# Kernel tuning notes

Measured on AMD Instinct MI355X. Metric: run time of the kernel, lower is better.

## Reference

```python
import jax, jax.numpy as jnp
import numpy as np

# Module hyperparameters (from init_kwargs)
LEARNING_RATE = 0.01  # not used inside compute_weight_update
TAU_PLUS = 20.0
TAU_MINUS = 20.0
A_PLUS = 0.005
A_MINUS = 0.00525
TARGET_RATE = 0.1
HOMEOSTATIC_RATE = 0.001
TAU_HOMEOSTATIC = 1000.0

B, T, N_PRE, N_POST = 16, 8192, 128, 128


def setup_inputs() -> dict:
    key = jax.random.key(0)
    k1, k2, k3 = jax.random.split(key, 3)
    # Bernoulli spike trains at ~target_rate firing probability
    pre_spikes = (jax.random.uniform(k1, (B, T, N_PRE)) < TARGET_RATE).astype(jnp.float32)
    post_spikes = (jax.random.uniform(k2, (B, T, N_POST)) < TARGET_RATE).astype(jnp.float32)
    weights = jax.random.uniform(k3, (N_PRE, N_POST), dtype=jnp.float32)
    return {"pre_spikes": pre_spikes, "post_spikes": post_spikes, "weights": weights, "dt": 1}


def _temporal_corr(x, kernel, pad):
    """Correlate x [B,T,N] along time with 1-D kernel [L], padding pad=(lo,hi)."""
    b, t, n = x.shape
    xr = jnp.moveaxis(x, 1, 2).reshape(b * n, 1, t)  # [B*N, 1, T]
    k = kernel.reshape(1, 1, -1).astype(x.dtype)
    y = jax.lax.conv_general_dilated(
        xr, k, window_strides=(1,), padding=[pad],
        dimension_numbers=("NCH", "OIH", "NCH"))
    return jnp.moveaxis(y.reshape(b, n, t), 2, 1)  # [B,T,N]


def reference(pre_spikes, post_spikes, weights, dt):
    b, t, n_pre = pre_spikes.shape
    dt = float(dt)

    # Homeostatic rate tracking (first call: avg rates initialized to target_rate)
    alpha = dt / TAU_HOMEOSTATIC
    current_post_rate = post_spikes.mean(axis=(0, 1))
    avg_post_rate = (1.0 - alpha) * TARGET_RATE + alpha * current_post_rate

    # Truncated exponential STDP window: tau in 1..min(int(3*tau)-1, ...) = 1..59
    L = int(TAU_PLUS * 3)  # 60 taps (tau=0 tap zeroed)
    taus = jnp.arange(L, dtype=jnp.float32)
    w_plus = jnp.where(taus > 0, A_PLUS * jnp.exp(-taus * dt / TAU_PLUS), 0.0)
    w_minus = jnp.where(taus > 0, A_MINUS * jnp.exp(-taus * dt / TAU_MINUS), 0.0)

    # LTP: post_filt[t] = sum_{tau>=1} w_plus[tau] * post[t+tau] (future, zero-padded)
    post_filt = _temporal_corr(post_spikes, w_plus, (0, L - 1))
    # LTD: pre_filt[t] = sum_{tau>=1} w_minus[tau] * pre[t-tau] (past, zero-padded)
    pre_filt = _temporal_corr(pre_spikes, w_minus[::-1], (L - 1, 0))

    # sum_t mean_b outer(pre[t], post_filt[t]) - outer(pre_filt[t], post[t]), then /T
    ltp = jnp.einsum("btp,btq->pq", pre_spikes, post_filt)
    ltd = jnp.einsum("btp,btq->pq", pre_filt, post_spikes)
    stdp_update = (ltp - ltd) / (b * t)

    # Homeostatic regulation pulls post rate toward target
    post_rate_error = avg_post_rate - TARGET_RATE
    homeostatic_update = -HOMEOSTATIC_RATE * post_rate_error[None, :] * weights

    return stdp_update + homeostatic_update
```

## Files before the change

kernel.cpp:

```cpp
#include <hip/hip_runtime.h>

#define BB 16
#define TT 8192
#define NN 128
constexpr int CHUNK = 256;
constexpr int NBLK  = BB * TT / CHUNK;
constexpr int OUTN  = NN * NN;
constexpr int GS    = 264;
constexpr int SLOTS = OUTN / 2;
constexpr int PROWS = 315;

typedef _Float16 f16x8 __attribute__((ext_vector_type(8)));
typedef _Float16 f16x2 __attribute__((ext_vector_type(2)));
typedef float    f32x4 __attribute__((ext_vector_type(4)));

__device__ __forceinline__ unsigned short h16(float x) {
    _Float16 h = (_Float16)x;
    return __builtin_bit_cast(unsigned short, h);
}
__device__ __forceinline__ unsigned int pack2(float x, float y) {
    return (unsigned int)h16(x) | ((unsigned int)h16(y) << 16);
}
__device__ __forceinline__ float2 ldL(const unsigned short* p_lds, int m, int q0) {
    const unsigned int v = *(const unsigned int*)&p_lds[m * NN + q0];
    const f16x2 h = __builtin_bit_cast(f16x2, v);
    return make_float2((float)h[0], (float)h[1]);
}

template<bool ATOMIC>
__global__ __launch_bounds__(512, 4)
void stdp_main(const float* __restrict__ pre, const float* __restrict__ post,
               const int* __restrict__ dtp,
               unsigned int* __restrict__ part, float* __restrict__ wpost,
               float* __restrict__ outat)
{
    __shared__ __align__(16) char smem[PROWS * NN * 2];
    unsigned short* post_lds = (unsigned short*)smem;
    unsigned short* g_lds    = (unsigned short*)smem;
    float*          lds_ps   = (float*)(smem + NN * GS * 2);

    const int tid   = threadIdx.x;
    const int blk   = blockIdx.x;
    const int b     = blk >> 5;
    const int chunk = blk & 31;
    const int t0    = chunk * CHUNK;
    const int wv    = tid >> 6;
    const int lane  = tid & 63;

    const float dtf = (float)(*dtp);
    const float r   = expf(-dtf * (1.0f / 20.0f));

    const float* pb = post + (size_t)b * TT * NN;
    const float* ab = pre  + (size_t)b * TT * NN;

    {
        const int c  = tid & 31;
        const int mr = tid >> 5;
        for (int m = mr; m < PROWS; m += 16) {
            const int t = t0 + 1 + m;
            float4 v = make_float4(0.f, 0.f, 0.f, 0.f);
            if (t < TT) v = *(const float4*)(pb + (size_t)t * NN + c * 4);
            *(uint2*)&post_lds[m * NN + c * 4] = make_uint2(pack2(v.x, v.y), pack2(v.z, v.w));
        }
    }
    __syncthreads();

    const int win  = wv;
    const int q0   = lane * 2;
    const int base = win * 32;
    float ps0 = 0.f, ps1 = 0.f;

    unsigned int pk0[16], pk1[16];
    {
        float2 p  = ldL(post_lds, base + 31, q0);
        float wt  = r;
        float gx = r * p.x, gy = r * p.y;
        ps0 += p.x; ps1 += p.y;
        #pragma unroll
        for (int tau = 2; tau <= 59; ++tau) {
            wt *= r;
            p = ldL(post_lds, base + 30 + tau, q0);
            gx = fmaf(wt, p.x, gx);
            gy = fmaf(wt, p.y, gy);
        }
        const float r60 = wt * r;
        pk0[15] = (unsigned int)h16(gx) << 16;
        pk1[15] = (unsigned int)h16(gy) << 16;
        #pragma unroll
        for (int c = 30; c >= 0; --c) {
            const float2 p1  = ldL(post_lds, base + c,      q0);
            const float2 p60 = ldL(post_lds, base + c + 59, q0);
            gx = r * (gx + p1.x) - r60 * p60.x;
            gy = r * (gy + p1.y) - r60 * p60.y;
            ps0 += p1.x; ps1 += p1.y;
            if (c & 1) {
                pk0[c >> 1] = (unsigned int)h16(gx) << 16;
                pk1[c >> 1] = (unsigned int)h16(gy) << 16;
            } else {
                pk0[c >> 1] |= h16(gx);
                pk1[c >> 1] |= h16(gy);
            }
        }
    }
    __syncthreads();

    {
        unsigned short* d0 = &g_lds[q0 * GS + win * 32];
        unsigned short* d1 = &g_lds[(q0 + 1) * GS + win * 32];
        #pragma unroll
        for (int s = 0; s < 4; ++s) {
            *(uint4*)(d0 + 8 * s) = make_uint4(pk0[4*s], pk0[4*s+1], pk0[4*s+2], pk0[4*s+3]);
            *(uint4*)(d1 + 8 * s) = make_uint4(pk1[4*s], pk1[4*s+1], pk1[4*s+2], pk1[4*s+3]);
        }
        lds_ps[win * NN + q0]     = ps0;
        lds_ps[win * NN + q0 + 1] = ps1;
    }
    __syncthreads();

    if (tid < NN) {
        float s = 0.f;
        #pragma unroll
        for (int w = 0; w < 8; ++w) s += lds_ps[w * NN + tid];
        if (chunk == 0) s += pb[tid];
        if constexpr (ATOMIC) atomicAdd(&wpost[tid], s);
        else wpost[(size_t)tid * NBLK + blk] = s;
    }

    const int pr0 = wv * 16;
    f32x4 acc[8];
    #pragma unroll
    for (int qt = 0; qt < 8; ++qt) acc[qt] = (f32x4){0.f, 0.f, 0.f, 0.f};

    const float* abase = ab + (size_t)(t0 + (lane >> 4) * 8) * NN + pr0 + (lane & 15);
    float an[8];
    #pragma unroll
    for (int j = 0; j < 8; ++j) an[j] = abase[(size_t)j * NN];

    #pragma unroll
    for (int ks = 0; ks < 8; ++ks) {
        f16x8 af;
        #pragma unroll
        for (int j = 0; j < 8; ++j) af[j] = (_Float16)an[j];
        if (ks < 7) {
            const float* src = abase + (size_t)((ks + 1) * 32) * NN;
            #pragma unroll
            for (int j = 0; j < 8; ++j) an[j] = src[(size_t)j * NN];
        }
        const int koff = ks * 32 + (lane >> 4) * 8;
        #pragma unroll
        for (int qt = 0; qt < 8; ++qt) {
            const f16x8 bf = *(const f16x8*)&g_lds[(qt * 16 + (lane & 15)) * GS + koff];
            acc[qt] = __builtin_amdgcn_mfma_f32_16x16x32_f16(af, bf, acc[qt], 0, 0, 0);
        }
    }

    if constexpr (!ATOMIC) {
        unsigned int* dst = part + ((size_t)blk * 8 + wv) * 1024 + lane;
        #pragma unroll
        for (int qt = 0; qt < 8; ++qt)
            #pragma unroll
            for (int rp = 0; rp < 2; ++rp)
                dst[qt * 128 + rp * 64] = pack2(acc[qt][2 * rp], acc[qt][2 * rp + 1]);
    } else {
        #pragma unroll
        for (int qt = 0; qt < 8; ++qt)
            #pragma unroll
            for (int rg = 0; rg < 4; ++rg) {
                const int prow = pr0 + (lane >> 4) * 4 + rg;
                const int qcol = qt * 16 + (lane & 15);
                atomicAdd(&outat[prow * NN + qcol], acc[qt][rg]);
            }
    }
}

__global__ __launch_bounds__(512)
void finalize_ws(const unsigned int* __restrict__ part, const float* __restrict__ wpost,
                 const int* __restrict__ dtp, const float* __restrict__ W,
                 float* __restrict__ out)
{
    __shared__ float2 red[512];
    __shared__ float  hfs[16];
    const int s    = threadIdx.x & 63;
    const int kq   = threadIdx.x >> 6;
    const int slot = blockIdx.x * 64 + s;
    const int qt   = (slot >> 7) & 7;
    const int qbase = qt * 16;

    {
        const int qi   = threadIdx.x >> 5;
        const int part5 = threadIdx.x & 31;
        float hsum = 0.f;
        const float* wq = wpost + (size_t)(qbase + qi) * NBLK;
        #pragma unroll
        for (int k = part5; k < NBLK; k += 32) hsum += wq[k];
        #pragma unroll
        for (int off = 16; off; off >>= 1) hsum += __shfl_down(hsum, off, 32);
        if (part5 == 0) {
            const float dtf   = (float)(*dtp);
            const float alpha = dtf * 1e-3f;
            hfs[qi] = -0.001f * (alpha * (hsum * (1.0f / (float)(BB * TT)) - 0.1f));
        }
    }

    float sx = 0.f, sy = 0.f;
    #pragma unroll 8
    for (int k = kq * 64; k < kq * 64 + 64; ++k) {
        const unsigned int v = part[(size_t)k * SLOTS + slot];
        const f16x2 h = __builtin_bit_cast(f16x2, v);
        sx += (float)h[0];
        sy += (float)h[1];
    }
    red[threadIdx.x] = make_float2(sx, sy);
    __syncthreads();
    if (threadIdx.x < 64) {
        float tx = red[s].x, ty = red[s].y;
        #pragma unroll
        for (int g = 1; g < 8; ++g) {
            const float2 v = red[g * 64 + s];
            tx += v.x; ty += v.y;
        }
        const int lane = slot & 63;
        const int rp   = (slot >> 6) & 1;
        const int wv   = slot >> 10;
        const int p    = wv * 16 + ((lane >> 4) << 2) + rp * 2;
        const int qi   = lane & 15;
        const int q    = qbase + qi;
        const float scale = (float)((0.005 - 0.00525) / (double)(BB * TT));
        const float hf = hfs[qi];
        out[p * NN + q]       = fmaf(tx, scale, hf * W[p * NN + q]);
        out[(p + 1) * NN + q] = fmaf(ty, scale, hf * W[(p + 1) * NN + q]);
    }
}

__global__ void finalize_at(const float* __restrict__ wpost, const int* __restrict__ dtp,
                            const float* __restrict__ W, float* __restrict__ out)
{
    const int i = (blockIdx.x * 256 + threadIdx.x) * 2;
    const int q = i & 127;
    const float scale = (float)((0.005 - 0.00525) / (double)(BB * TT));
    const float dtf   = (float)(*dtp);
    const float alpha = dtf * 1e-3f;
    const float inv   = 1.0f / (float)(BB * TT);
    const float hf0   = -0.001f * (alpha * (wpost[q]     * inv - 0.1f));
    const float hf1   = -0.001f * (alpha * (wpost[q + 1] * inv - 0.1f));
    float2 sv = *(const float2*)(out + i);
    float2 w  = *(const float2*)(W + i);
    float2 o;
    o.x = fmaf(sv.x, scale, hf0 * w.x);
    o.y = fmaf(sv.y, scale, hf1 * w.y);
    *(float2*)(out + i) = o;
}

extern "C" void kernel_launch(void* const* d_in, const int* in_sizes, int n_in,
                              void* d_out, int out_size, void* d_ws, size_t ws_size,
                              hipStream_t stream)
{
    const float* pre  = (const float*)d_in[0];
    const float* post = (const float*)d_in[1];
    const float* W    = (const float*)d_in[2];
    const int*   dtp  = (const int*)d_in[3];
    float* out = (float*)d_out;

    const size_t part_bytes  = (size_t)NBLK * SLOTS * sizeof(unsigned int);
    const size_t wpost_bytes = (size_t)NN * NBLK * sizeof(float);
    const size_t need = part_bytes + wpost_bytes;

    if (ws_size >= need) {
        unsigned int* part = (unsigned int*)d_ws;
        float* wpost       = (float*)((char*)d_ws + part_bytes);
        hipLaunchKernelGGL((stdp_main<false>), dim3(NBLK), dim3(512), 0, stream,
                           pre, post, dtp, part, wpost, (float*)nullptr);
        hipLaunchKernelGGL(finalize_ws, dim3(SLOTS / 64), dim3(512), 0, stream,
                           part, wpost, dtp, W, out);
    } else {
        float* wpost = (float*)d_ws;
        hipMemsetAsync(d_out, 0, OUTN * sizeof(float), stream);
        hipMemsetAsync(wpost, 0, NN * sizeof(float), stream);
        hipLaunchKernelGGL((stdp_main<true>), dim3(NBLK), dim3(512), 0, stream,
                           pre, post, dtp, (unsigned int*)nullptr, wpost, out);
        hipLaunchKernelGGL(finalize_at, dim3(OUTN / 512), dim3(256), 0, stream,
                           wpost, dtp, W, out);
    }
}
```

Measured before the change: 165.9 us.

## Process two time chunks per block with prefetched post rows and split LDS

Each block now handles two consecutive 256-step chunks instead of one, halving the grid and the number of partial-sum tiles written and reduced by the finalize kernel. The second chunk's post-spike rows are prefetched into registers while the first chunk's filter runs. The filter input and output now live in separate LDS buffers, so the second chunk's filter can reuse the first chunk's MFMA accumulators. This costs more LDS and registers, occupancy drops to 2 blocks per CU, and the serial work per block grows.

```diff
diff --git a/kernel.cpp b/kernel.cpp
--- a/kernel.cpp
+++ b/kernel.cpp
@@ -4,7 +4,8 @@
 #define TT 8192
 #define NN 128
 constexpr int CHUNK = 256;
-constexpr int NBLK  = BB * TT / CHUNK;
+constexpr int NCH   = BB * TT / CHUNK;
+constexpr int NBLK  = NCH / 2;
 constexpr int OUTN  = NN * NN;
 constexpr int GS    = 264;
 constexpr int SLOTS = OUTN / 2;
@@ -28,24 +29,25 @@
 }
 
 template<bool ATOMIC>
-__global__ __launch_bounds__(512, 4)
+__global__ __launch_bounds__(512, 2)
 void stdp_main(const float* __restrict__ pre, const float* __restrict__ post,
                const int* __restrict__ dtp,
                unsigned int* __restrict__ part, float* __restrict__ wpost,
                float* __restrict__ outat)
 {
-    __shared__ __align__(16) char smem[PROWS * NN * 2];
-    unsigned short* post_lds = (unsigned short*)smem;
-    unsigned short* g_lds    = (unsigned short*)smem;
-    float*          lds_ps   = (float*)(smem + NN * GS * 2);
-
-    const int tid   = threadIdx.x;
-    const int blk   = blockIdx.x;
-    const int b     = blk >> 5;
-    const int chunk = blk & 31;
-    const int t0    = chunk * CHUNK;
-    const int wv    = tid >> 6;
-    const int lane  = tid & 63;
+    __shared__ __align__(16) unsigned short bufP[PROWS * NN];
+    __shared__ __align__(16) unsigned short bufG[NN * GS];
+    __shared__ float lds_ps[8 * NN];
+
+    const int tid    = threadIdx.x;
+    const int bi     = blockIdx.x;
+    const int c0g    = bi * 2;
+    const int b      = c0g >> 5;
+    const int chunk0 = c0g & 31;
+    const int t00    = chunk0 * CHUNK;
+    const int t01    = t00 + CHUNK;
+    const int wv     = tid >> 6;
+    const int lane   = tid & 63;
 
     const float dtf = (float)(*dtp);
     const float r   = expf(-dtf * (1.0f / 20.0f));
@@ -53,77 +55,93 @@
     const float* pb = post + (size_t)b * TT * NN;
     const float* ab = pre  + (size_t)b * TT * NN;
 
-    {
-        const int c  = tid & 31;
-        const int mr = tid >> 5;
-        for (int m = mr; m < PROWS; m += 16) {
-            const int t = t0 + 1 + m;
-            float4 v = make_float4(0.f, 0.f, 0.f, 0.f);
-            if (t < TT) v = *(const float4*)(pb + (size_t)t * NN + c * 4);
-            *(uint2*)&post_lds[m * NN + c * 4] = make_uint2(pack2(v.x, v.y), pack2(v.z, v.w));
-        }
-    }
-    __syncthreads();
-
-    const int win  = wv;
-    const int q0   = lane * 2;
-    const int base = win * 32;
-    float ps0 = 0.f, ps1 = 0.f;
+    const int sc = tid & 31;
+    const int mr = tid >> 5;
+
+    for (int m = mr; m < PROWS; m += 16) {
+        const int t = t00 + 1 + m;
+        const float4 v = *(const float4*)(pb + (size_t)t * NN + sc * 4);
+        *(uint2*)&bufP[m * NN + sc * 4] = make_uint2(pack2(v.x, v.y), pack2(v.z, v.w));
+    }
+    __syncthreads();
+
+    float4 va[20];
+    #pragma unroll
+    for (int i = 0; i < 20; ++i) {
+        const int m = mr + i * 16;
+        const int t = t01 + 1 + m;
+        va[i] = make_float4(0.f, 0.f, 0.f, 0.f);
+        if (m < PROWS && t < TT) va[i] = *(const float4*)(pb + (size_t)t * NN + sc * 4);
+    }
+
+    const int q0 = lane * 2;
 
     unsigned int pk0[16], pk1[16];
-    {
-        float2 p  = ldL(post_lds, base + 31, q0);
-        float wt  = r;
-        float gx = r * p.x, gy = r * p.y;
-        ps0 += p.x; ps1 += p.y;
-        #pragma unroll
-        for (int tau = 2; tau <= 59; ++tau) {
-            wt *= r;
-            p = ldL(post_lds, base + 30 + tau, q0);
-            gx = fmaf(wt, p.x, gx);
-            gy = fmaf(wt, p.y, gy);
-        }
-        const float r60 = wt * r;
-        pk0[15] = (unsigned int)h16(gx) << 16;
-        pk1[15] = (unsigned int)h16(gy) << 16;
-        #pragma unroll
-        for (int c = 30; c >= 0; --c) {
-            const float2 p1  = ldL(post_lds, base + c,      q0);
-            const float2 p60 = ldL(post_lds, base + c + 59, q0);
-            gx = r * (gx + p1.x) - r60 * p60.x;
-            gy = r * (gy + p1.y) - r60 * p60.y;
-            ps0 += p1.x; ps1 += p1.y;
-            if (c & 1) {
-                pk0[c >> 1] = (unsigned int)h16(gx) << 16;
-                pk1[c >> 1] = (unsigned int)h16(gy) << 16;
-            } else {
-                pk0[c >> 1] |= h16(gx);
-                pk1[c >> 1] |= h16(gy);
-            }
-        }
-    }
-    __syncthreads();
-
-    {
-        unsigned short* d0 = &g_lds[q0 * GS + win * 32];
-        unsigned short* d1 = &g_lds[(q0 + 1) * GS + win * 32];
-        #pragma unroll
-        for (int s = 0; s < 4; ++s) {
-            *(uint4*)(d0 + 8 * s) = make_uint4(pk0[4*s], pk0[4*s+1], pk0[4*s+2], pk0[4*s+3]);
-            *(uint4*)(d1 + 8 * s) = make_uint4(pk1[4*s], pk1[4*s+1], pk1[4*s+2], pk1[4*s+3]);
-        }
-        lds_ps[win * NN + q0]     = ps0;
-        lds_ps[win * NN + q0 + 1] = ps1;
-    }
-    __syncthreads();
+    float ps0, ps1;
+    #define FILTER_PHASE(SRC) {                                               \
+        const int base = wv * 32;                                             \
+        ps0 = 0.f; ps1 = 0.f;                                                 \
+        float2 p  = ldL(SRC, base + 31, q0);                                  \
+        float wt  = r;                                                        \
+        float gx = r * p.x, gy = r * p.y;                                     \
+        ps0 += p.x; ps1 += p.y;                                               \
+        _Pragma("unroll")                                                     \
+        for (int tau = 2; tau <= 59; ++tau) {                                 \
+            wt *= r;                                                          \
+            p = ldL(SRC, base + 30 + tau, q0);                                \
+            gx = fmaf(wt, p.x, gx);                                           \
+            gy = fmaf(wt, p.y, gy);                                           \
+        }                                                                     \
+        const float r60 = wt * r;                                             \
+        pk0[15] = (unsigned int)h16(gx) << 16;                                \
+        pk1[15] = (unsigned int)h16(gy) << 16;                                \
+        _Pragma("unroll")                                                     \
+        for (int c = 30; c >= 0; --c) {                                       \
+            const float2 p1  = ldL(SRC, base + c,      q0);                   \
+            const float2 p60 = ldL(SRC, base + c + 59, q0);                   \
+            gx = r * (gx + p1.x) - r60 * p60.x;                               \
+            gy = r * (gy + p1.y) - r60 * p60.y;                               \
+            ps0 += p1.x; ps1 += p1.y;                                         \
+            if (c & 1) {                                                      \
+                pk0[c >> 1] = (unsigned int)h16(gx) << 16;                    \
+                pk1[c >> 1] = (unsigned int)h16(gy) << 16;                    \
+            } else {                                                          \
+                pk0[c >> 1] |= h16(gx);                                       \
+                pk1[c >> 1] |= h16(gy);                                       \
+            }                                                                 \
+        }                                                                     \
+    }
+    #define DUMP_G() {                                                        \
+        unsigned short* d0 = &bufG[q0 * GS + wv * 32];                        \
+        unsigned short* d1 = &bufG[(q0 + 1) * GS + wv * 32];                  \
+        _Pragma("unroll")                                                     \
+        for (int s = 0; s < 4; ++s) {                                         \
+            *(uint4*)(d0 + 8*s) = make_uint4(pk0[4*s], pk0[4*s+1], pk0[4*s+2], pk0[4*s+3]); \
+            *(uint4*)(d1 + 8*s) = make_uint4(pk1[4*s], pk1[4*s+1], pk1[4*s+2], pk1[4*s+3]); \
+        }                                                                     \
+        lds_ps[wv * NN + q0]     = ps0;                                       \
+        lds_ps[wv * NN + q0 + 1] = ps1;                                       \
+    }
+
+    FILTER_PHASE(bufP)
+    DUMP_G()
+    __syncthreads();
+
+    #pragma unroll
+    for (int i = 0; i < 20; ++i) {
+        const int m = mr + i * 16;
+        if (m < PROWS)
+            *(uint2*)&bufP[m * NN + sc * 4] =
+                make_uint2(pack2(va[i].x, va[i].y), pack2(va[i].z, va[i].w));
+    }
 
     if (tid < NN) {
         float s = 0.f;
         #pragma unroll
         for (int w = 0; w < 8; ++w) s += lds_ps[w * NN + tid];
-        if (chunk == 0) s += pb[tid];
+        if (chunk0 == 0) s += pb[tid];
         if constexpr (ATOMIC) atomicAdd(&wpost[tid], s);
-        else wpost[(size_t)tid * NBLK + blk] = s;
+        else wpost[(size_t)tid * NCH + c0g] = s;
     }
 
     const int pr0 = wv * 16;
@@ -131,31 +149,49 @@
     #pragma unroll
     for (int qt = 0; qt < 8; ++qt) acc[qt] = (f32x4){0.f, 0.f, 0.f, 0.f};
 
-    const float* abase = ab + (size_t)(t0 + (lane >> 4) * 8) * NN + pr0 + (lane & 15);
-    float an[8];
-    #pragma unroll
-    for (int j = 0; j < 8; ++j) an[j] = abase[(size_t)j * NN];
-
-    #pragma unroll
-    for (int ks = 0; ks < 8; ++ks) {
-        f16x8 af;
-        #pragma unroll
-        for (int j = 0; j < 8; ++j) af[j] = (_Float16)an[j];
-        if (ks < 7) {
-            const float* src = abase + (size_t)((ks + 1) * 32) * NN;
-            #pragma unroll
-            for (int j = 0; j < 8; ++j) an[j] = src[(size_t)j * NN];
-        }
-        const int koff = ks * 32 + (lane >> 4) * 8;
-        #pragma unroll
-        for (int qt = 0; qt < 8; ++qt) {
-            const f16x8 bf = *(const f16x8*)&g_lds[(qt * 16 + (lane & 15)) * GS + koff];
-            acc[qt] = __builtin_amdgcn_mfma_f32_16x16x32_f16(af, bf, acc[qt], 0, 0, 0);
-        }
-    }
+    #define MFMA_PHASE(T0) {                                                  \
+        const float* abase = ab + (size_t)((T0) + (lane >> 4) * 8) * NN + pr0 + (lane & 15); \
+        float an[8];                                                          \
+        _Pragma("unroll")                                                     \
+        for (int j = 0; j < 8; ++j) an[j] = abase[(size_t)j * NN];            \
+        _Pragma("unroll")                                                     \
+        for (int ks = 0; ks < 8; ++ks) {                                      \
+            f16x8 af;                                                         \
+            _Pragma("unroll")                                                 \
+            for (int j = 0; j < 8; ++j) af[j] = (_Float16)an[j];              \
+            if (ks < 7) {                                                     \
+                const float* src = abase + (size_t)((ks + 1) * 32) * NN;      \
+                _Pragma("unroll")                                             \
+                for (int j = 0; j < 8; ++j) an[j] = src[(size_t)j * NN];      \
+            }                                                                 \
+            const int koff = ks * 32 + (lane >> 4) * 8;                       \
+            _Pragma("unroll")                                                 \
+            for (int qt = 0; qt < 8; ++qt) {                                  \
+                const f16x8 bf = *(const f16x8*)&bufG[(qt * 16 + (lane & 15)) * GS + koff]; \
+                acc[qt] = __builtin_amdgcn_mfma_f32_16x16x32_f16(af, bf, acc[qt], 0, 0, 0); \
+            }                                                                 \
+        }                                                                     \
+    }
+
+    MFMA_PHASE(t00)
+    __syncthreads();
+
+    FILTER_PHASE(bufP)
+    DUMP_G()
+    __syncthreads();
+
+    if (tid < NN) {
+        float s = 0.f;
+        #pragma unroll
+        for (int w = 0; w < 8; ++w) s += lds_ps[w * NN + tid];
+        if constexpr (ATOMIC) atomicAdd(&wpost[tid], s);
+        else wpost[(size_t)tid * NCH + c0g + 1] = s;
+    }
+
+    MFMA_PHASE(t01)
 
     if constexpr (!ATOMIC) {
-        unsigned int* dst = part + ((size_t)blk * 8 + wv) * 1024 + lane;
+        unsigned int* dst = part + ((size_t)bi * 8 + wv) * 1024 + lane;
         #pragma unroll
         for (int qt = 0; qt < 8; ++qt)
             #pragma unroll
@@ -171,6 +207,9 @@
                 atomicAdd(&outat[prow * NN + qcol], acc[qt][rg]);
             }
     }
+    #undef FILTER_PHASE
+    #undef DUMP_G
+    #undef MFMA_PHASE
 }
 
 __global__ __launch_bounds__(512)
@@ -187,15 +226,15 @@
     const int qbase = qt * 16;
 
     {
-        const int qi   = threadIdx.x >> 5;
-        const int part5 = threadIdx.x & 31;
+        const int qi = threadIdx.x >> 5;
+        const int pr = threadIdx.x & 31;
         float hsum = 0.f;
-        const float* wq = wpost + (size_t)(qbase + qi) * NBLK;
-        #pragma unroll
-        for (int k = part5; k < NBLK; k += 32) hsum += wq[k];
+        const float* wq = wpost + (size_t)(qbase + qi) * NCH;
+        #pragma unroll 4
+        for (int k = pr; k < NCH; k += 32) hsum += wq[k];
         #pragma unroll
         for (int off = 16; off; off >>= 1) hsum += __shfl_down(hsum, off, 32);
-        if (part5 == 0) {
+        if (pr == 0) {
             const float dtf   = (float)(*dtp);
             const float alpha = dtf * 1e-3f;
             hfs[qi] = -0.001f * (alpha * (hsum * (1.0f / (float)(BB * TT)) - 0.1f));
@@ -204,7 +243,7 @@
 
     float sx = 0.f, sy = 0.f;
     #pragma unroll 8
-    for (int k = kq * 64; k < kq * 64 + 64; ++k) {
+    for (int k = kq * (NBLK / 8); k < (kq + 1) * (NBLK / 8); ++k) {
         const unsigned int v = part[(size_t)k * SLOTS + slot];
         const f16x2 h = __builtin_bit_cast(f16x2, v);
         sx += (float)h[0];
@@ -262,7 +301,7 @@
     float* out = (float*)d_out;
 
     const size_t part_bytes  = (size_t)NBLK * SLOTS * sizeof(unsigned int);
-    const size_t wpost_bytes = (size_t)NN * NBLK * sizeof(float);
+    const size_t wpost_bytes = (size_t)NN * NCH * sizeof(float);
     const size_t need = part_bytes + wpost_bytes;
 
     if (ws_size >= need) {
```

Measured after the change: 158.8 us, median of 2. -4.3%, faster.

## Process two time chunks per block with separate LDS buffers and prefetch

Applied to the files above, without the earlier changes.

Each block now handles two consecutive 256-step chunks, keeping MFMA accumulators across both. This halves the number of partial tiles written to and reduced from the workspace. Post-spike tile and filtered tile get separate LDS buffers, so the second chunk's post load overlaps the first chunk's store phase. The cost is more LDS per block (lower occupancy), half as many blocks, and a serialized per-block loop.

```diff
diff --git a/kernel.cpp b/kernel.cpp
--- a/kernel.cpp
+++ b/kernel.cpp
@@ -4,7 +4,8 @@
 #define TT 8192
 #define NN 128
 constexpr int CHUNK = 256;
-constexpr int NBLK  = BB * TT / CHUNK;
+constexpr int NCH   = BB * TT / CHUNK;
+constexpr int NBLK  = NCH / 2;
 constexpr int OUTN  = NN * NN;
 constexpr int GS    = 264;
 constexpr int SLOTS = OUTN / 2;
@@ -34,18 +35,18 @@
                unsigned int* __restrict__ part, float* __restrict__ wpost,
                float* __restrict__ outat)
 {
-    __shared__ __align__(16) char smem[PROWS * NN * 2];
-    unsigned short* post_lds = (unsigned short*)smem;
-    unsigned short* g_lds    = (unsigned short*)smem;
-    float*          lds_ps   = (float*)(smem + NN * GS * 2);
-
-    const int tid   = threadIdx.x;
-    const int blk   = blockIdx.x;
-    const int b     = blk >> 5;
-    const int chunk = blk & 31;
-    const int t0    = chunk * CHUNK;
-    const int wv    = tid >> 6;
-    const int lane  = tid & 63;
+    __shared__ __align__(16) unsigned short bufP[PROWS * NN];
+    __shared__ __align__(16) unsigned short bufG[NN * GS];
+    __shared__ float lds_ps[8 * NN];
+
+    const int tid    = threadIdx.x;
+    const int bi     = blockIdx.x;
+    const int c0g    = bi * 2;
+    const int b      = c0g >> 5;
+    const int chunk0 = c0g & 31;
+    const int t00    = chunk0 * CHUNK;
+    const int wv     = tid >> 6;
+    const int lane   = tid & 63;
 
     const float dtf = (float)(*dtp);
     const float r   = expf(-dtf * (1.0f / 20.0f));
@@ -53,109 +54,121 @@
     const float* pb = post + (size_t)b * TT * NN;
     const float* ab = pre  + (size_t)b * TT * NN;
 
-    {
-        const int c  = tid & 31;
-        const int mr = tid >> 5;
-        for (int m = mr; m < PROWS; m += 16) {
-            const int t = t0 + 1 + m;
-            float4 v = make_float4(0.f, 0.f, 0.f, 0.f);
-            if (t < TT) v = *(const float4*)(pb + (size_t)t * NN + c * 4);
-            *(uint2*)&post_lds[m * NN + c * 4] = make_uint2(pack2(v.x, v.y), pack2(v.z, v.w));
-        }
+    const int sc = tid & 31;
+    const int mr = tid >> 5;
+    const int q0 = lane * 2;
+
+    for (int m = mr; m < PROWS; m += 16) {
+        const int t = t00 + 1 + m;
+        const float4 v = *(const float4*)(pb + (size_t)t * NN + sc * 4);
+        *(uint2*)&bufP[m * NN + sc * 4] = make_uint2(pack2(v.x, v.y), pack2(v.z, v.w));
     }
     __syncthreads();
 
-    const int win  = wv;
-    const int q0   = lane * 2;
-    const int base = win * 32;
-    float ps0 = 0.f, ps1 = 0.f;
-
-    unsigned int pk0[16], pk1[16];
-    {
-        float2 p  = ldL(post_lds, base + 31, q0);
-        float wt  = r;
-        float gx = r * p.x, gy = r * p.y;
-        ps0 += p.x; ps1 += p.y;
-        #pragma unroll
-        for (int tau = 2; tau <= 59; ++tau) {
-            wt *= r;
-            p = ldL(post_lds, base + 30 + tau, q0);
-            gx = fmaf(wt, p.x, gx);
-            gy = fmaf(wt, p.y, gy);
-        }
-        const float r60 = wt * r;
-        pk0[15] = (unsigned int)h16(gx) << 16;
-        pk1[15] = (unsigned int)h16(gy) << 16;
-        #pragma unroll
-        for (int c = 30; c >= 0; --c) {
-            const float2 p1  = ldL(post_lds, base + c,      q0);
-            const float2 p60 = ldL(post_lds, base + c + 59, q0);
-            gx = r * (gx + p1.x) - r60 * p60.x;
-            gy = r * (gy + p1.y) - r60 * p60.y;
-            ps0 += p1.x; ps1 += p1.y;
-            if (c & 1) {
-                pk0[c >> 1] = (unsigned int)h16(gx) << 16;
-                pk1[c >> 1] = (unsigned int)h16(gy) << 16;
-            } else {
-                pk0[c >> 1] |= h16(gx);
-                pk1[c >> 1] |= h16(gy);
-            }
-        }
-    }
-    __syncthreads();
-
-    {
-        unsigned short* d0 = &g_lds[q0 * GS + win * 32];
-        unsigned short* d1 = &g_lds[(q0 + 1) * GS + win * 32];
-        #pragma unroll
-        for (int s = 0; s < 4; ++s) {
-            *(uint4*)(d0 + 8 * s) = make_uint4(pk0[4*s], pk0[4*s+1], pk0[4*s+2], pk0[4*s+3]);
-            *(uint4*)(d1 + 8 * s) = make_uint4(pk1[4*s], pk1[4*s+1], pk1[4*s+2], pk1[4*s+3]);
-        }
-        lds_ps[win * NN + q0]     = ps0;
-        lds_ps[win * NN + q0 + 1] = ps1;
-    }
-    __syncthreads();
-
-    if (tid < NN) {
-        float s = 0.f;
-        #pragma unroll
-        for (int w = 0; w < 8; ++w) s += lds_ps[w * NN + tid];
-        if (chunk == 0) s += pb[tid];
-        if constexpr (ATOMIC) atomicAdd(&wpost[tid], s);
-        else wpost[(size_t)tid * NBLK + blk] = s;
-    }
-
-    const int pr0 = wv * 16;
     f32x4 acc[8];
     #pragma unroll
     for (int qt = 0; qt < 8; ++qt) acc[qt] = (f32x4){0.f, 0.f, 0.f, 0.f};
 
-    const float* abase = ab + (size_t)(t0 + (lane >> 4) * 8) * NN + pr0 + (lane & 15);
-    float an[8];
-    #pragma unroll
-    for (int j = 0; j < 8; ++j) an[j] = abase[(size_t)j * NN];
-
-    #pragma unroll
-    for (int ks = 0; ks < 8; ++ks) {
-        f16x8 af;
-        #pragma unroll
-        for (int j = 0; j < 8; ++j) af[j] = (_Float16)an[j];
-        if (ks < 7) {
-            const float* src = abase + (size_t)((ks + 1) * 32) * NN;
-            #pragma unroll
-            for (int j = 0; j < 8; ++j) an[j] = src[(size_t)j * NN];
-        }
-        const int koff = ks * 32 + (lane >> 4) * 8;
-        #pragma unroll
-        for (int qt = 0; qt < 8; ++qt) {
-            const f16x8 bf = *(const f16x8*)&g_lds[(qt * 16 + (lane & 15)) * GS + koff];
-            acc[qt] = __builtin_amdgcn_mfma_f32_16x16x32_f16(af, bf, acc[qt], 0, 0, 0);
+    const int pr0 = wv * 16;
+
+    #pragma unroll 1
+    for (int cc = 0; cc < 2; ++cc) {
+        const int t0 = t00 + cc * CHUNK;
+
+        const int base = wv * 32;
+        float ps0 = 0.f, ps1 = 0.f;
+        unsigned int pk0[16], pk1[16];
+        {
+            float2 p  = ldL(bufP, base + 31, q0);
+            float wt  = r;
+            float gx = r * p.x, gy = r * p.y;
+            ps0 += p.x; ps1 += p.y;
+            #pragma unroll 2
+            for (int tau = 2; tau <= 59; ++tau) {
+                wt *= r;
+                p = ldL(bufP, base + 30 + tau, q0);
+                gx = fmaf(wt, p.x, gx);
+                gy = fmaf(wt, p.y, gy);
+            }
+            const float r60 = wt * r;
+            pk0[15] = (unsigned int)h16(gx) << 16;
+            pk1[15] = (unsigned int)h16(gy) << 16;
+            #pragma unroll
+            for (int c = 30; c >= 0; --c) {
+                const float2 p1  = ldL(bufP, base + c,      q0);
+                const float2 p60 = ldL(bufP, base + c + 59, q0);
+                gx = r * (gx + p1.x) - r60 * p60.x;
+                gy = r * (gy + p1.y) - r60 * p60.y;
+                ps0 += p1.x; ps1 += p1.y;
+                if (c & 1) {
+                    pk0[c >> 1] = (unsigned int)h16(gx) << 16;
+                    pk1[c >> 1] = (unsigned int)h16(gy) << 16;
+                } else {
+                    pk0[c >> 1] |= h16(gx);
+                    pk1[c >> 1] |= h16(gy);
+                }
+            }
+        }
+        __syncthreads();
+
+        {
+            unsigned short* d0 = &bufG[q0 * GS + base];
+            unsigned short* d1 = &bufG[(q0 + 1) * GS + base];
+            #pragma unroll
+            for (int s = 0; s < 4; ++s) {
+                *(uint4*)(d0 + 8*s) = make_uint4(pk0[4*s], pk0[4*s+1], pk0[4*s+2], pk0[4*s+3]);
+                *(uint4*)(d1 + 8*s) = make_uint4(pk1[4*s], pk1[4*s+1], pk1[4*s+2], pk1[4*s+3]);
+            }
+            lds_ps[wv * NN + q0]     = ps0;
+            lds_ps[wv * NN + q0 + 1] = ps1;
+        }
+
+        if (cc == 0) {
+            for (int m = mr; m < PROWS; m += 16) {
+                const int t = t00 + CHUNK + 1 + m;
+                float4 v = make_float4(0.f, 0.f, 0.f, 0.f);
+                if (t < TT) v = *(const float4*)(pb + (size_t)t * NN + sc * 4);
+                *(uint2*)&bufP[m * NN + sc * 4] = make_uint2(pack2(v.x, v.y), pack2(v.z, v.w));
+            }
+        }
+        __syncthreads();
+
+        if (tid < NN) {
+            float s = 0.f;
+            #pragma unroll
+            for (int w = 0; w < 8; ++w) s += lds_ps[w * NN + tid];
+            if (chunk0 == 0 && cc == 0) s += pb[tid];
+            if constexpr (ATOMIC) atomicAdd(&wpost[tid], s);
+            else wpost[(size_t)tid * NCH + c0g + cc] = s;
+        }
+
+        {
+            const float* abase = ab + (size_t)(t0 + (lane >> 4) * 8) * NN + pr0 + (lane & 15);
+            float an[8];
+            #pragma unroll
+            for (int j = 0; j < 8; ++j) an[j] = abase[(size_t)j * NN];
+            #pragma unroll
+            for (int ks = 0; ks < 8; ++ks) {
+                f16x8 af;
+                #pragma unroll
+                for (int j = 0; j < 8; ++j) af[j] = (_Float16)an[j];
+                if (ks < 7) {
+                    const float* src = abase + (size_t)((ks + 1) * 32) * NN;
+                    #pragma unroll
+                    for (int j = 0; j < 8; ++j) an[j] = src[(size_t)j * NN];
+                }
+                const int koff = ks * 32 + (lane >> 4) * 8;
+                #pragma unroll
+                for (int qt = 0; qt < 8; ++qt) {
+                    const f16x8 bf = *(const f16x8*)&bufG[(qt * 16 + (lane & 15)) * GS + koff];
+                    acc[qt] = __builtin_amdgcn_mfma_f32_16x16x32_f16(af, bf, acc[qt], 0, 0, 0);
+                }
+            }
         }
     }
 
     if constexpr (!ATOMIC) {
-        unsigned int* dst = part + ((size_t)blk * 8 + wv) * 1024 + lane;
+        unsigned int* dst = part + ((size_t)bi * 8 + wv) * 1024 + lane;
         #pragma unroll
         for (int qt = 0; qt < 8; ++qt)
             #pragma unroll
@@ -187,15 +200,15 @@
     const int qbase = qt * 16;
 
     {
-        const int qi   = threadIdx.x >> 5;
-        const int part5 = threadIdx.x & 31;
+        const int qi = threadIdx.x >> 5;
+        const int pr = threadIdx.x & 31;
         float hsum = 0.f;
-        const float* wq = wpost + (size_t)(qbase + qi) * NBLK;
-        #pragma unroll
-        for (int k = part5; k < NBLK; k += 32) hsum += wq[k];
+        const float* wq = wpost + (size_t)(qbase + qi) * NCH;
+        #pragma unroll 4
+        for (int k = pr; k < NCH; k += 32) hsum += wq[k];
         #pragma unroll
         for (int off = 16; off; off >>= 1) hsum += __shfl_down(hsum, off, 32);
-        if (part5 == 0) {
+        if (pr == 0) {
             const float dtf   = (float)(*dtp);
             const float alpha = dtf * 1e-3f;
             hfs[qi] = -0.001f * (alpha * (hsum * (1.0f / (float)(BB * TT)) - 0.1f));
@@ -204,7 +217,7 @@
 
     float sx = 0.f, sy = 0.f;
     #pragma unroll 8
-    for (int k = kq * 64; k < kq * 64 + 64; ++k) {
+    for (int k = kq * (NBLK / 8); k < (kq + 1) * (NBLK / 8); ++k) {
         const unsigned int v = part[(size_t)k * SLOTS + slot];
         const f16x2 h = __builtin_bit_cast(f16x2, v);
         sx += (float)h[0];
@@ -262,7 +275,7 @@
     float* out = (float*)d_out;
 
     const size_t part_bytes  = (size_t)NBLK * SLOTS * sizeof(unsigned int);
-    const size_t wpost_bytes = (size_t)NN * NBLK * sizeof(float);
+    const size_t wpost_bytes = (size_t)NN * NCH * sizeof(float);
     const size_t need = part_bytes + wpost_bytes;
 
     if (ws_size >= need) {
```

New measurement: 167.4 us. Within noise of the previous version (+0.9%).
